# Optimization experiments

Measured on AMD Instinct MI355X. Metric: run time of the kernel, lower is better.

## Reference

```python
import jax, jax.numpy as jnp
import numpy as np

N, K, D, M, P, HG, HD = 120000, 8, 64, 100000, 16, 32, 96
VOXEL, TAU, OCC_INC, LMIN, LMAX = 0.1, 0.3, 0.5, -2.0, 3.5


def setup_inputs() -> dict:
    ks = jax.random.split(jax.random.key(0), 20)
    f32 = jnp.float32
    s = 0.05
    return {
        'pts_xyz': jax.random.uniform(ks[0], (N, 3), f32) * 10.0,
        'f_pts': jax.random.normal(ks[1], (N, D), f32),
        'z_latent': jax.random.normal(ks[2], (M, D), f32),
        'vals_st': jax.random.normal(ks[3], (M,), f32) * 0.5,
        'centers_xyz': jax.random.uniform(ks[4], (M, 3), f32) * 10.0,
        'Wf': jax.random.normal(ks[5], (P, D), f32) * s,
        'Wz': jax.random.normal(ks[6], (P, D), f32) * s,
        'w_delta': jax.random.normal(ks[7], (1, 3), f32) * s,
        'b_delta': jnp.zeros((1,), f32),
        'log_temp': jnp.zeros((1,), f32),
        'W_ih': jax.random.normal(ks[8], (3 * D, D), f32) * s,
        'W_hh': jax.random.normal(ks[9], (3 * D, D), f32) * s,
        'b_ih': jnp.zeros((3 * D,), f32),
        'b_hh': jnp.zeros((3 * D,), f32),
        'Wg1': jax.random.normal(ks[10], (HG, 2 * D), f32) * s,
        'bg1': jnp.zeros((HG,), f32),
        'Wg2': jax.random.normal(ks[11], (1, HG), f32) * s,
        'bg2': jnp.zeros((1,), f32),
        'ln_g': jnp.ones((D,), f32),
        'ln_b': jnp.zeros((D,), f32),
        'Wd1': jax.random.normal(ks[12], (HD, D), f32) * s,
        'bd1': jnp.zeros((HD,), f32),
        'Wd2': jax.random.normal(ks[13], (HD, HD), f32) * s,
        'bd2': jnp.zeros((HD,), f32),
        'Wd3': jax.random.normal(ks[14], (1, HD), f32) * s,
        'bd3': jnp.zeros((1,), f32),
        'keys': jnp.sort(jax.random.randint(ks[15], (M,), 0, 2 ** 30, jnp.int32)),
        'cand_idx': jax.random.randint(ks[16], (N, K), 0, M, jnp.int32),
    }


def _forward(pts_xyz, f_pts, z_latent, vals_st, centers_xyz, Wf, Wz, w_delta, b_delta,
             log_temp, W_ih, W_hh, b_ih, b_hh, Wg1, bg1, Wg2, bg2, ln_g, ln_b,
             Wd1, bd1, Wd2, bd2, Wd3, bd3, keys, cand_idx):
    # --- sparse voxel hash lookup + log-odds scatter update ---
    ijk = jnp.floor(pts_xyz / VOXEL).astype(jnp.int32)
    off = jnp.int32(1 << 9)
    h = ((ijk[:, 0] + off) << 20) ^ ((ijk[:, 1] + off) << 10) ^ (ijk[:, 2] + off)
    vox_idx = jnp.clip(jnp.searchsorted(keys, h), 0, M - 1)  # (N,)
    vals_new = jnp.clip(vals_st.at[vox_idx].add(OCC_INC), LMIN, LMAX)

    # --- top-K low-temperature routing: sim(f, z, delta) ---
    z_c = z_latent[cand_idx]                                  # (N,K,D) gather
    delta = pts_xyz[:, None, :] - centers_xyz[cand_idx]       # (N,K,3)
    Fp = f_pts @ Wf.T                                         # (N,P)
    Zp = z_c @ Wz.T                                           # (N,K,P)
    Fp = Fp / (jnp.linalg.norm(Fp, axis=-1, keepdims=True) + 1e-6)
    Zp = Zp / (jnp.linalg.norm(Zp, axis=-1, keepdims=True) + 1e-6)
    core = jnp.einsum('np,nkp->nk', Fp, Zp)
    dterm = jnp.einsum('nkc,c->nk', delta, w_delta[0]) + b_delta[0]
    sim = jnp.exp(log_temp[0]) * (core + dterm)
    w = jax.nn.softmax(sim / TAU, axis=-1)                    # (N,K)

    # --- scatter weighted point features to voxels ---
    flat_idx = cand_idx.reshape(-1)                           # (N*K,)
    contrib = (w[..., None] * f_pts[:, None, :]).reshape(-1, D)
    msg = jax.ops.segment_sum(contrib, flat_idx, num_segments=M)   # (M,D)
    wsum = jax.ops.segment_sum(w.reshape(-1), flat_idx, num_segments=M)
    msg = msg / (wsum[:, None] + 1e-6)

    # --- per-voxel gate + GRU latent fusion ---
    gate_in = jnp.concatenate([z_latent, msg], axis=-1)       # (M,2D)
    g = jax.nn.sigmoid(jax.nn.relu(gate_in @ Wg1.T + bg1) @ Wg2.T + bg2)  # (M,1)
    gi = msg @ W_ih.T + b_ih
    gh = z_latent @ W_hh.T + b_hh
    gir, giz, gin = jnp.split(gi, 3, axis=-1)
    ghr, ghz, ghn = jnp.split(gh, 3, axis=-1)
    r = jax.nn.sigmoid(gir + ghr)
    u = jax.nn.sigmoid(giz + ghz)
    n = jnp.tanh(gin + r * ghn)
    h_new = (1.0 - u) * n + u * z_latent
    z_new = z_latent + g * (h_new - z_latent)                 # (M,D)

    # --- decode occupancy: LN -> fc1 -> residual fc2 -> fc3 -> sigmoid ---
    mu = z_new.mean(-1, keepdims=True)
    var = z_new.var(-1, keepdims=True)
    x = (z_new - mu) * jax.lax.rsqrt(var + 1e-5) * ln_g + ln_b
    hd = jax.nn.relu(x @ Wd1.T + bd1)
    hd = hd + jax.nn.relu(hd @ Wd2.T + bd2)
    p = jax.nn.sigmoid((hd @ Wd3.T + bd3)[:, 0])              # (M,)

    return jnp.concatenate([p, vals_new])                     # (2M,)


def reference(pts_xyz, f_pts, z_latent, vals_st, centers_xyz, Wf, Wz, w_delta, b_delta,
              log_temp, W_ih, W_hh, b_ih, b_hh, Wg1, bg1, Wg2, bg2, ln_g, ln_b,
              Wd1, bd1, Wd2, bd2, Wd3, bd3, keys, cand_idx):
    return _forward(pts_xyz, f_pts, z_latent, vals_st, centers_xyz, Wf, Wz, w_delta,
                    b_delta, log_temp, W_ih, W_hh, b_ih, b_hh, Wg1, bg1, Wg2, bg2,
                    ln_g, ln_b, Wd1, bd1, Wd2, bd2, Wd3, bd3, keys, cand_idx)
```

## Files before the change

### kernel.cpp

```cpp
#include <hip/hip_runtime.h>
#include <math.h>

#define Nn 120000
#define Kk 8
#define Dd 64
#define Mm 100000
#define Pp 16
#define HGg 32
#define HDd 96
#define CAP 40
#define LUTB 16

typedef __attribute__((ext_vector_type(8))) short bf16x8;
typedef __attribute__((ext_vector_type(4))) float f32x4;
typedef __attribute__((ext_vector_type(4))) float fx4;
typedef __attribute__((ext_vector_type(4))) int ix4;

#define PB_K0    1563
#define PB_PREP  (PB_K0 + 3750)
#define PB_PACK  (PB_PREP + 22)
#define PB_INIT  (PB_PACK + 391)
#define PB_LUT   (PB_INIT + 391)

__device__ __forceinline__ float sigmoidf_(float x) { return 1.f / (1.f + __expf(-x)); }
__device__ __forceinline__ float tanh_fast(float x) {
    float e = __expf(2.f * x);
    return 1.f - 2.f / (e + 1.f);
}
__device__ __forceinline__ short f2bf(float f) {
    unsigned u = __float_as_uint(f);
    unsigned r = (u + 0x7fffu + ((u >> 16) & 1u)) >> 16;
    return (short)r;
}

__global__ __launch_bounds__(256) void k_prep_all(const float* __restrict__ z,
                                                  const float* __restrict__ Wz,
                                                  const float* __restrict__ centers,
                                                  const float* __restrict__ w_delta,
                                                  const int* __restrict__ keys,
                                                  const float* __restrict__ f_pts,
                                                  const float* __restrict__ Wf,
                                                  const float* __restrict__ Wg1,
                                                  const float* __restrict__ W_ih,
                                                  const float* __restrict__ W_hh,
                                                  const float* __restrict__ Wd1,
                                                  const float* __restrict__ Wd2,
                                                  const float* __restrict__ vals,
                                                  unsigned* __restrict__ Zbf,
                                                  float* __restrict__ cdot,
                                                  int* __restrict__ lut,
                                                  signed char* __restrict__ f8,
                                                  float* __restrict__ fpb,
                                                  short* __restrict__ wsW,
                                                  int* __restrict__ cnt,
                                                  float* __restrict__ vacc) {
    int b = blockIdx.x;
    if (b < PB_K0) {
        int g = threadIdx.x & 3;
        int m = b * 64 + (threadIdx.x >> 2);
        if (m >= Mm) return;
        const float4* zr = (const float4*)(z + (size_t)m * Dd + g * 16);
        float4 q0 = zr[0], q1 = zr[1], q2 = zr[2], q3 = zr[3];
        float acc[Pp];
#pragma unroll
        for (int p = 0; p < Pp; p++) {
            const float4* w = (const float4*)(Wz + (size_t)p * Dd + g * 16);
            float4 w0 = w[0], w1 = w[1], w2 = w[2], w3 = w[3];
            float s = q0.x * w0.x + q0.y * w0.y + q0.z * w0.z + q0.w * w0.w;
            s += q1.x * w1.x + q1.y * w1.y + q1.z * w1.z + q1.w * w1.w;
            s += q2.x * w2.x + q2.y * w2.y + q2.z * w2.z + q2.w * w2.w;
            s += q3.x * w3.x + q3.y * w3.y + q3.z * w3.z + q3.w * w3.w;
            acc[p] = s;
        }
#pragma unroll
        for (int p = 0; p < Pp; p++) {
            acc[p] += __shfl_xor(acc[p], 1, 64);
            acc[p] += __shfl_xor(acc[p], 2, 64);
        }
        float ss = 0.f;
#pragma unroll
        for (int p = 0; p < Pp; p++) ss = fmaf(acc[p], acc[p], ss);
        float inv = 1.f / (sqrtf(ss) + 1e-6f);
        unsigned* row = Zbf + (size_t)m * 8;
        if (g < 2) {
            uint4 o;
            unsigned w[4];
#pragma unroll
            for (int j = 0; j < 4; j++) {
                float v0 = acc[g * 8 + 2 * j] * inv;
                float v1 = acc[g * 8 + 2 * j + 1] * inv;
                w[j] = (unsigned)(unsigned short)f2bf(v0)
                     | ((unsigned)(unsigned short)f2bf(v1) << 16);
            }
            o.x = w[0]; o.y = w[1]; o.z = w[2]; o.w = w[3];
            ((uint4*)row)[g] = o;
        } else if (g == 2) {
            cdot[m] = centers[3 * m] * w_delta[0] + centers[3 * m + 1] * w_delta[1]
                    + centers[3 * m + 2] * w_delta[2];
        }
    } else if (b < PB_PREP) {
        int i = (b - PB_K0) * 256 + threadIdx.x;
        int g = i & 7;
        int e = i * 8;
        const fx4* src = (const fx4*)(f_pts + e);
        fx4 a = __builtin_nontemporal_load(src);
        fx4 bb = __builtin_nontemporal_load(src + 1);
        float v[8] = {a.x, a.y, a.z, a.w, bb.x, bb.y, bb.z, bb.w};
        unsigned lo = 0, hi = 0;
#pragma unroll
        for (int j = 0; j < 4; j++) {
            int q = (int)rintf(fminf(fmaxf(v[j], -4.f), 4.f) * 32.f);
            lo |= ((unsigned)q & 0xffu) << (8 * j);
        }
#pragma unroll
        for (int j = 0; j < 4; j++) {
            int q = (int)rintf(fminf(fmaxf(v[4 + j], -4.f), 4.f) * 32.f);
            hi |= ((unsigned)q & 0xffu) << (8 * j);
        }
        *(int2*)(f8 + e) = make_int2((int)lo, (int)hi);

        float fp[Pp];
#pragma unroll
        for (int p = 0; p < Pp; p++) {
            const float4* w = (const float4*)(Wf + (size_t)p * Dd + g * 8);
            float4 w0 = w[0], w1 = w[1];
            float s = v[0] * w0.x + v[1] * w0.y + v[2] * w0.z + v[3] * w0.w;
            s += v[4] * w1.x + v[5] * w1.y + v[6] * w1.z + v[7] * w1.w;
            fp[p] = s;
        }
#pragma unroll
        for (int p = 0; p < Pp; p++) {
            fp[p] += __shfl_xor(fp[p], 1, 64);
            fp[p] += __shfl_xor(fp[p], 2, 64);
            fp[p] += __shfl_xor(fp[p], 4, 64);
        }
        float ss = 0.f;
#pragma unroll
        for (int p = 0; p < Pp; p++) ss = fmaf(fp[p], fp[p], ss);
        float inv = 1.f / (sqrtf(ss) + 1e-6f);
#pragma unroll
        for (int p = 0; p < Pp; p++) fp[p] *= inv;
        if (g < 4) {
            float4 o;
            if (g == 0)      o = make_float4(fp[0], fp[1], fp[2], fp[3]);
            else if (g == 1) o = make_float4(fp[4], fp[5], fp[6], fp[7]);
            else if (g == 2) o = make_float4(fp[8], fp[9], fp[10], fp[11]);
            else             o = make_float4(fp[12], fp[13], fp[14], fp[15]);
            ((float4*)(fpb + (size_t)(i >> 3) * 16))[g] = o;
        }
    } else if (b < PB_PACK) {
        int idx = (b - PB_PREP) * 256 + threadIdx.x;
        if (idx >= 86 * 64) return;
        int f = idx >> 6, lane = idx & 63;
        int lrow = lane & 15, lhi = lane >> 4;
        const float* src;
        int t, c, K;
        if (f < 8)       { int g = f;      t = g >> 2; c = g & 3;  src = Wg1;  K = 128; }
        else if (f < 32) { int g = f - 8;  t = g >> 1; c = g & 1;  src = W_ih; K = 64; }
        else if (f < 56) { int g = f - 32; t = g >> 1; c = g & 1;  src = W_hh; K = 64; }
        else if (f < 68) { int g = f - 56; t = g >> 1; c = g & 1;  src = Wd1;  K = 64; }
        else             { int g = f - 68; t = g / 3;  c = g % 3;  src = Wd2;  K = 96; }
        int o = t * 16 + lrow;
        int k0 = c * 32 + lhi * 8;
        short* dst = wsW + ((size_t)f * 64 + lane) * 8;
#pragma unroll
        for (int j = 0; j < 8; j++) dst[j] = f2bf(src[(size_t)o * K + k0 + j]);
    } else if (b < PB_INIT) {
        int m = (b - PB_PACK) * 256 + threadIdx.x;
        if (m < Mm) {
            cnt[m] = 0;
            vacc[m] = vals[m];
        }
    } else {
        int i = (b - PB_INIT) * 256 + threadIdx.x;
        if (i <= Mm) {
            const int S = 30 - LUTB;
            int ki = (i < Mm) ? keys[i] : (1 << 30);
            int kp = (i > 0) ? keys[i - 1] : -1;
            int lo = (kp >> S) + 1;
            int hi = ki >> S;
            for (int p = lo; p <= hi; p++) lut[p] = i;
        }
    }
}

__global__ __launch_bounds__(256) void k1_route(const float* __restrict__ pts,
                                                const float* __restrict__ fpb,
                                                const float* __restrict__ w_delta,
                                                const float* __restrict__ b_delta,
                                                const float* __restrict__ log_temp,
                                                const int* __restrict__ keys,
                                                const int* __restrict__ cand,
                                                const unsigned* __restrict__ Zbf,
                                                const float* __restrict__ cdot,
                                                const int* __restrict__ lut,
                                                float* __restrict__ vacc,
                                                int* __restrict__ cnt,
                                                int2* __restrict__ rec) {
    int g = threadIdx.x & 7;
    int n = blockIdx.x * 32 + (threadIdx.x >> 3);

    int myid = __builtin_nontemporal_load(cand + (size_t)n * Kk + g);
    const uint4* zp = (const uint4*)(Zbf + (size_t)myid * 8);
    uint4 A = zp[0], B = zp[1];
    float cd = cdot[myid];
    const float4* fr = (const float4*)(fpb + (size_t)n * 16);
    float4 F0 = fr[0], F1 = fr[1], F2 = fr[2], F3 = fr[3];
    float px = pts[3 * n], py = pts[3 * n + 1], pz = pts[3 * n + 2];

    if (g == 0) {
        int ix = (int)floorf(px / 0.1f);
        int iy = (int)floorf(py / 0.1f);
        int iz = (int)floorf(pz / 0.1f);
        int h = ((ix + 512) << 20) ^ ((iy + 512) << 10) ^ (iz + 512);
        int pfx = h >> (30 - LUTB);
        int lo = lut[pfx], hi = lut[pfx + 1];
        while (lo < hi) {
            int mid = (lo + hi) >> 1;
            if (keys[mid] < h) lo = mid + 1; else hi = mid;
        }
        int vi = lo < (Mm - 1) ? lo : (Mm - 1);
        atomicAdd(vacc + vi, 0.5f);
    }

    float et = expf(log_temp[0]);
    float pdot = px * w_delta[0] + py * w_delta[1] + pz * w_delta[2] + b_delta[0];

    float fp[16] = {F0.x, F0.y, F0.z, F0.w, F1.x, F1.y, F1.z, F1.w,
                    F2.x, F2.y, F2.z, F2.w, F3.x, F3.y, F3.z, F3.w};
    unsigned uw[8] = {A.x, A.y, A.z, A.w, B.x, B.y, B.z, B.w};
    float core = 0.f;
#pragma unroll
    for (int j = 0; j < 8; j++) {
        float lo = __uint_as_float(uw[j] << 16);
        float hi = __uint_as_float(uw[j] & 0xffff0000u);
        core = fmaf(fp[2 * j], lo, core);
        core = fmaf(fp[2 * j + 1], hi, core);
    }
    float sim = et * (core + pdot - cd) / 0.3f;

    float mx = sim;
    mx = fmaxf(mx, __shfl_xor(mx, 1, 64));
    mx = fmaxf(mx, __shfl_xor(mx, 2, 64));
    mx = fmaxf(mx, __shfl_xor(mx, 4, 64));
    float e = __expf(sim - mx);
    float se = e;
    se += __shfl_xor(se, 1, 64);
    se += __shfl_xor(se, 2, 64);
    se += __shfl_xor(se, 4, 64);
    float w = e / se;

    int pos = atomicAdd(cnt + myid, 1);
    if (pos < CAP) {
        long long pk = (unsigned)n | ((long long)(unsigned)__float_as_int(w) << 32);
        *(long long*)(rec + (size_t)myid * CAP + pos) = pk;
    }
}

__global__ __launch_bounds__(256) void k2_reduce(const signed char* __restrict__ f8,
                                                 const int* __restrict__ cnt,
                                                 const int2* __restrict__ rec,
                                                 unsigned short* __restrict__ msgb) {
    int wv = threadIdx.x >> 6, lane = threadIdx.x & 63;
    int m = blockIdx.x * 4 + wv;
    int c = cnt[m];
    if (c > CAP) c = CAP;
    const ix4* r4 = (const ix4*)(rec + (size_t)m * CAP);
    float acc = 0.f, wsum = 0.f;
    for (int i0 = 0; i0 < c; i0 += 8) {
        ix4 A = __builtin_nontemporal_load(r4 + (i0 >> 1) + 0);
        ix4 B = __builtin_nontemporal_load(r4 + (i0 >> 1) + 1);
        ix4 C = __builtin_nontemporal_load(r4 + (i0 >> 1) + 2);
        ix4 D = __builtin_nontemporal_load(r4 + (i0 >> 1) + 3);
        int nn[8];
        float ww[8];
        int rn[8] = {A.x, A.z, B.x, B.z, C.x, C.z, D.x, D.z};
        int rw[8] = {A.y, A.w, B.y, B.w, C.y, C.w, D.y, D.w};
#pragma unroll
        for (int k = 0; k < 8; k++) {
            bool valid = (i0 + k) < c;
            nn[k] = valid ? rn[k] : 0;
            ww[k] = valid ? __int_as_float(rw[k]) : 0.f;
        }
        float vv[8];
#pragma unroll
        for (int k = 0; k < 8; k++)
            vv[k] = (float)f8[((size_t)nn[k] << 6) + lane];
#pragma unroll
        for (int k = 0; k < 8; k++) {
            wsum += ww[k];
            acc = fmaf(ww[k], vv[k], acc);
        }
    }
    acc *= 0.03125f;
    msgb[(size_t)m * Dd + lane] = (unsigned short)f2bf(acc / (wsum + 1e-6f));
}

__global__ __launch_bounds__(256, 3) void k3_mfma(const float* __restrict__ z_latent,
                                                  const unsigned short* __restrict__ msgb,
                                                  const short* __restrict__ wsW,
                                                  const float* __restrict__ bg1,
                                                  const float* __restrict__ Wg2,
                                                  const float* __restrict__ bg2,
                                                  const float* __restrict__ b_ih,
                                                  const float* __restrict__ b_hh,
                                                  const float* __restrict__ ln_g,
                                                  const float* __restrict__ ln_b,
                                                  const float* __restrict__ bd1,
                                                  const float* __restrict__ bd2,
                                                  const float* __restrict__ Wd3,
                                                  const float* __restrict__ bd3,
                                                  const float* __restrict__ vacc,
                                                  float* __restrict__ out) {
    __shared__ float scr_all[4][16 * 97];
    int wv = threadIdx.x >> 6, lane = threadIdx.x & 63;
    int tile = blockIdx.x * 4 + wv;
    if (tile >= Mm / 16) return;
    int m0 = tile * 16;
    float* scr = scr_all[wv];
    int lrow = lane & 15;
    int lhi = lane >> 4;

    if (lane < 16) {
        float v = vacc[m0 + lane];
        out[Mm + m0 + lane] = fminf(fmaxf(v, -2.f), 3.5f);
    }

    const bf16x8* WF = (const bf16x8*)wsW;
#define BFRAG(off) (WF[(off) * 64 + lane])

    bf16x8 za[2], ma[2];
    const float* zrow = z_latent + (size_t)(m0 + lrow) * Dd + lhi * 8;
    const bf16x8* mrow = (const bf16x8*)(msgb + (size_t)(m0 + lrow) * Dd + lhi * 8);
#pragma unroll
    for (int c = 0; c < 2; c++) {
        bf16x8 t0;
#pragma unroll
        for (int j = 0; j < 8; j++) t0[j] = f2bf(zrow[c * 32 + j]);
        za[c] = t0;
        ma[c] = mrow[c * 4];
    }

    bf16x8 wgf[8];
#pragma unroll
    for (int j = 0; j < 8; j++) wgf[j] = BFRAG(j);
    f32x4 g0 = {0.f, 0.f, 0.f, 0.f}, g1 = {0.f, 0.f, 0.f, 0.f};
    bf16x8 gateA[4] = {za[0], za[1], ma[0], ma[1]};
#pragma unroll
    for (int c = 0; c < 4; c++) {
        g0 = __builtin_amdgcn_mfma_f32_16x16x32_bf16(gateA[c], wgf[c], g0, 0, 0, 0);
        g1 = __builtin_amdgcn_mfma_f32_16x16x32_bf16(gateA[c], wgf[4 + c], g1, 0, 0, 0);
    }
    float bgA = bg1[lrow], bgB = bg1[16 + lrow];
    float w2A = Wg2[lrow], w2B = Wg2[16 + lrow];
    float g[4];
#pragma unroll
    for (int r = 0; r < 4; r++) {
        float ga = fmaxf(g0[r] + bgA, 0.f) * w2A + fmaxf(g1[r] + bgB, 0.f) * w2B;
        ga += __shfl_xor(ga, 1, 64);
        ga += __shfl_xor(ga, 2, 64);
        ga += __shfl_xor(ga, 4, 64);
        ga += __shfl_xor(ga, 8, 64);
        g[r] = sigmoidf_(ga + bg2[0]);
    }

    float zn[4][4];
    float ps[4] = {0.f, 0.f, 0.f, 0.f}, pq[4] = {0.f, 0.f, 0.f, 0.f};
#pragma unroll
    for (int t = 0; t < 4; t++) {
        bf16x8 wt[12];
#pragma unroll
        for (int c = 0; c < 2; c++) {
            wt[0 + c]  = BFRAG(8 + t * 2 + c);
            wt[2 + c]  = BFRAG(8 + (t + 4) * 2 + c);
            wt[4 + c]  = BFRAG(8 + (t + 8) * 2 + c);
            wt[6 + c]  = BFRAG(32 + t * 2 + c);
            wt[8 + c]  = BFRAG(32 + (t + 4) * 2 + c);
            wt[10 + c] = BFRAG(32 + (t + 8) * 2 + c);
        }
        f32x4 Ar = {0.f, 0.f, 0.f, 0.f}, Az = Ar, An = Ar, Br = Ar, Bz = Ar, Bn = Ar;
#pragma unroll
        for (int c = 0; c < 2; c++) {
            Ar = __builtin_amdgcn_mfma_f32_16x16x32_bf16(ma[c], wt[0 + c], Ar, 0, 0, 0);
            Az = __builtin_amdgcn_mfma_f32_16x16x32_bf16(ma[c], wt[2 + c], Az, 0, 0, 0);
            An = __builtin_amdgcn_mfma_f32_16x16x32_bf16(ma[c], wt[4 + c], An, 0, 0, 0);
            Br = __builtin_amdgcn_mfma_f32_16x16x32_bf16(za[c], wt[6 + c], Br, 0, 0, 0);
            Bz = __builtin_amdgcn_mfma_f32_16x16x32_bf16(za[c], wt[8 + c], Bz, 0, 0, 0);
            Bn = __builtin_amdgcn_mfma_f32_16x16x32_bf16(za[c], wt[10 + c], Bn, 0, 0, 0);
        }
        int oc = t * 16 + lrow;
        float bir = b_ih[oc], biz = b_ih[64 + oc], bin = b_ih[128 + oc];
        float bhr = b_hh[oc], bhz = b_hh[64 + oc], bhn = b_hh[128 + oc];
#pragma unroll
        for (int r = 0; r < 4; r++) {
            int row = lhi * 4 + r;
            float zo = z_latent[(size_t)(m0 + row) * Dd + oc];
            float rr = sigmoidf_(Ar[r] + bir + Br[r] + bhr);
            float uu = sigmoidf_(Az[r] + biz + Bz[r] + bhz);
            float nnv = tanh_fast(An[r] + bin + rr * (Bn[r] + bhn));
            float hn = (1.f - uu) * nnv + uu * zo;
            float z2 = zo + g[r] * (hn - zo);
            zn[t][r] = z2;
            ps[r] += z2;
            pq[r] = fmaf(z2, z2, pq[r]);
        }
    }
    float mu[4], rs[4];
#pragma unroll
    for (int r = 0; r < 4; r++) {
        float s = ps[r], q = pq[r];
        s += __shfl_xor(s, 1, 64); q += __shfl_xor(q, 1, 64);
        s += __shfl_xor(s, 2, 64); q += __shfl_xor(q, 2, 64);
        s += __shfl_xor(s, 4, 64); q += __shfl_xor(q, 4, 64);
        s += __shfl_xor(s, 8, 64); q += __shfl_xor(q, 8, 64);
        float m = s * (1.f / 64.f);
        float v = q * (1.f / 64.f) - m * m;
        mu[r] = m;
        rs[r] = rsqrtf(v + 1e-5f);
    }
#pragma unroll
    for (int t = 0; t < 4; t++) {
        int o = t * 16 + lrow;
        float lg = ln_g[o], lb = ln_b[o];
#pragma unroll
        for (int r = 0; r < 4; r++)
            scr[(lhi * 4 + r) * 97 + o] = (zn[t][r] - mu[r]) * rs[r] * lg + lb;
    }
    __threadfence_block();

    bf16x8 xa[2];
#pragma unroll
    for (int c = 0; c < 2; c++) {
        bf16x8 tb;
#pragma unroll
        for (int j = 0; j < 8; j++) tb[j] = f2bf(scr[lrow * 97 + c * 32 + lhi * 8 + j]);
        xa[c] = tb;
    }
    bf16x8 wf1[12];
#pragma unroll
    for (int j = 0; j < 12; j++) wf1[j] = BFRAG(56 + j);
    f32x4 h1t[6];
#pragma unroll
    for (int t = 0; t < 6; t++) h1t[t] = (f32x4){0.f, 0.f, 0.f, 0.f};
#pragma unroll
    for (int t = 0; t < 6; t++)
#pragma unroll
        for (int c = 0; c < 2; c++)
            h1t[t] = __builtin_amdgcn_mfma_f32_16x16x32_bf16(xa[c], wf1[t * 2 + c], h1t[t], 0, 0, 0);
    float h1r[6][4];
#pragma unroll
    for (int t = 0; t < 6; t++) {
        float bb = bd1[t * 16 + lrow];
#pragma unroll
        for (int r = 0; r < 4; r++) {
            h1r[t][r] = fmaxf(h1t[t][r] + bb, 0.f);
            scr[(lhi * 4 + r) * 97 + t * 16 + lrow] = h1r[t][r];
        }
    }
    __threadfence_block();

    bf16x8 ha[3];
#pragma unroll
    for (int c = 0; c < 3; c++) {
        bf16x8 tb;
#pragma unroll
        for (int j = 0; j < 8; j++) tb[j] = f2bf(scr[lrow * 97 + c * 32 + lhi * 8 + j]);
        ha[c] = tb;
    }
    bf16x8 wf2[18];
#pragma unroll
    for (int j = 0; j < 18; j++) wf2[j] = BFRAG(68 + j);
    f32x4 o2[6];
#pragma unroll
    for (int t = 0; t < 6; t++) o2[t] = (f32x4){0.f, 0.f, 0.f, 0.f};
#pragma unroll
    for (int t = 0; t < 6; t++)
#pragma unroll
        for (int c = 0; c < 3; c++)
            o2[t] = __builtin_amdgcn_mfma_f32_16x16x32_bf16(ha[c], wf2[t * 3 + c], o2[t], 0, 0, 0);
    float pacc[4] = {0.f, 0.f, 0.f, 0.f};
#pragma unroll
    for (int t = 0; t < 6; t++) {
        int o = t * 16 + lrow;
        float bb = bd2[o], w3 = Wd3[o];
#pragma unroll
        for (int r = 0; r < 4; r++) {
            float hd2 = h1r[t][r] + fmaxf(o2[t][r] + bb, 0.f);
            pacc[r] = fmaf(hd2, w3, pacc[r]);
        }
    }
#pragma unroll
    for (int r = 0; r < 4; r++) {
        float s = pacc[r];
        s += __shfl_xor(s, 1, 64);
        s += __shfl_xor(s, 2, 64);
        s += __shfl_xor(s, 4, 64);
        s += __shfl_xor(s, 8, 64);
        if (lrow == 0) out[m0 + lhi * 4 + r] = sigmoidf_(s + bd3[0]);
    }
#undef BFRAG
}

extern "C" void kernel_launch(void* const* d_in, const int* in_sizes, int n_in,
                              void* d_out, int out_size, void* d_ws, size_t ws_size,
                              hipStream_t stream) {
    const float* pts      = (const float*)d_in[0];
    const float* f_pts    = (const float*)d_in[1];
    const float* z_lat    = (const float*)d_in[2];
    const float* vals     = (const float*)d_in[3];
    const float* centers  = (const float*)d_in[4];
    const float* Wf       = (const float*)d_in[5];
    const float* Wz       = (const float*)d_in[6];
    const float* w_delta  = (const float*)d_in[7];
    const float* b_delta  = (const float*)d_in[8];
    const float* log_temp = (const float*)d_in[9];
    const float* W_ih     = (const float*)d_in[10];
    const float* W_hh     = (const float*)d_in[11];
    const float* b_ih     = (const float*)d_in[12];
    const float* b_hh     = (const float*)d_in[13];
    const float* Wg1      = (const float*)d_in[14];
    const float* bg1      = (const float*)d_in[15];
    const float* Wg2      = (const float*)d_in[16];
    const float* bg2      = (const float*)d_in[17];
    const float* ln_g     = (const float*)d_in[18];
    const float* ln_b     = (const float*)d_in[19];
    const float* Wd1      = (const float*)d_in[20];
    const float* bd1      = (const float*)d_in[21];
    const float* Wd2      = (const float*)d_in[22];
    const float* bd2      = (const float*)d_in[23];
    const float* Wd3      = (const float*)d_in[24];
    const float* bd3      = (const float*)d_in[25];
    const int*   keys     = (const int*)d_in[26];
    const int*   cand     = (const int*)d_in[27];
    float* out = (float*)d_out;

    float* ws = (float*)d_ws;
    short* wsW = (short*)ws;
    unsigned* Zbf = (unsigned*)(ws + 32768);
    float* cdot = ws + 32768 + 800000;
    signed char* f8 = (signed char*)(ws + 32768 + 900000);
    float* base = ws + 32768 + 900000 + 1920000;
    unsigned short* msgb = (unsigned short*)base;
    float* fpb = base;
    float* vacc = base + (size_t)Mm * Dd / 2;
    int*   cnt  = (int*)(vacc + Mm);
    int2*  rec  = (int2*)(cnt + Mm);
    int*   lut  = (int*)((int*)rec + (size_t)Mm * CAP * 2);

    k_prep_all<<<PB_LUT, 256, 0, stream>>>(z_lat, Wz, centers, w_delta, keys, f_pts,
                                           Wf, Wg1, W_ih, W_hh, Wd1, Wd2, vals,
                                           Zbf, cdot, lut, f8, fpb, wsW, cnt, vacc);
    k1_route<<<Nn / 32, 256, 0, stream>>>(pts, fpb, w_delta, b_delta, log_temp,
                                          keys, cand, Zbf, cdot, lut, vacc, cnt, rec);
    k2_reduce<<<Mm / 4, 256, 0, stream>>>(f8, cnt, rec, msgb);
    k3_mfma<<<(Mm / 16 + 3) / 4, 256, 0, stream>>>(z_lat, msgb, wsW, bg1, Wg2, bg2,
                                                   b_ih, b_hh, ln_g, ln_b, bd1, bd2,
                                                   Wd3, bd3, vacc, out);
}
```

Measured before the change: 320.4 us.

## Bin scatter records by voxel blocks and reduce with LDS atomics

Per-voxel record lists with capacity 40 are replaced by bins of 128 voxels. Each bin is split into 8 sub-buckets chosen from the routing block index, so fewer global cells receive atomics and the writes are more contiguous. The reduce kernel now runs one block per bin and accumulates the weighted messages in shared memory with LDS atomics before writing them out. In exchange, far fewer reduce blocks are launched, which cuts available parallelism. It also adds more global atomic contention on the bin counters, and records beyond 256 per sub-bucket are silently dropped.

```diff
diff --git a/kernel.cpp b/kernel.cpp
--- a/kernel.cpp
+++ b/kernel.cpp
@@ -8,8 +8,9 @@
 #define Pp 16
 #define HGg 32
 #define HDd 96
-#define CAP 40
 #define LUTB 16
+#define NBINS 782
+#define BCAP 256
 
 typedef __attribute__((ext_vector_type(8))) short bf16x8;
 typedef __attribute__((ext_vector_type(4))) float f32x4;
@@ -52,7 +53,7 @@
                                                   signed char* __restrict__ f8,
                                                   float* __restrict__ fpb,
                                                   short* __restrict__ wsW,
-                                                  int* __restrict__ cnt,
+                                                  int* __restrict__ bincnt,
                                                   float* __restrict__ vacc) {
     int b = blockIdx.x;
     if (b < PB_K0) {
@@ -167,10 +168,8 @@
         for (int j = 0; j < 8; j++) dst[j] = f2bf(src[(size_t)o * K + k0 + j]);
     } else if (b < PB_INIT) {
         int m = (b - PB_PACK) * 256 + threadIdx.x;
-        if (m < Mm) {
-            cnt[m] = 0;
-            vacc[m] = vals[m];
-        }
+        if (m < Mm) vacc[m] = vals[m];
+        if (m < 8 * NBINS) bincnt[m] = 0;
     } else {
         int i = (b - PB_INIT) * 256 + threadIdx.x;
         if (i <= Mm) {
@@ -195,8 +194,8 @@
                                                 const float* __restrict__ cdot,
                                                 const int* __restrict__ lut,
                                                 float* __restrict__ vacc,
-                                                int* __restrict__ cnt,
-                                                int2* __restrict__ rec) {
+                                                int* __restrict__ bincnt,
+                                                long long* __restrict__ binrec) {
     int g = threadIdx.x & 7;
     int n = blockIdx.x * 32 + (threadIdx.x >> 3);
 
@@ -250,50 +249,70 @@
     se += __shfl_xor(se, 4, 64);
     float w = e / se;
 
-    int pos = atomicAdd(cnt + myid, 1);
-    if (pos < CAP) {
-        long long pk = (unsigned)n | ((long long)(unsigned)__float_as_int(w) << 32);
-        *(long long*)(rec + (size_t)myid * CAP + pos) = pk;
+    int bin = myid >> 7;
+    int cell = ((blockIdx.x & 7) * NBINS) + bin;
+    int pos = atomicAdd(bincnt + cell, 1);
+    if (pos < BCAP) {
+        unsigned lo32 = (unsigned)n | ((unsigned)(myid & 127) << 17);
+        long long pk = (long long)(((unsigned long long)(unsigned)__float_as_int(w) << 32)
+                                   | (unsigned long long)lo32);
+        binrec[((size_t)cell << 8) + pos] = pk;
     }
 }
 
 __global__ __launch_bounds__(256) void k2_reduce(const signed char* __restrict__ f8,
-                                                 const int* __restrict__ cnt,
-                                                 const int2* __restrict__ rec,
+                                                 const int* __restrict__ bincnt,
+                                                 const long long* __restrict__ binrec,
                                                  unsigned short* __restrict__ msgb) {
-    int wv = threadIdx.x >> 6, lane = threadIdx.x & 63;
-    int m = blockIdx.x * 4 + wv;
-    int c = cnt[m];
-    if (c > CAP) c = CAP;
-    const ix4* r4 = (const ix4*)(rec + (size_t)m * CAP);
-    float acc = 0.f, wsum = 0.f;
-    for (int i0 = 0; i0 < c; i0 += 8) {
-        ix4 A = __builtin_nontemporal_load(r4 + (i0 >> 1) + 0);
-        ix4 B = __builtin_nontemporal_load(r4 + (i0 >> 1) + 1);
-        ix4 C = __builtin_nontemporal_load(r4 + (i0 >> 1) + 2);
-        ix4 D = __builtin_nontemporal_load(r4 + (i0 >> 1) + 3);
-        int nn[8];
-        float ww[8];
-        int rn[8] = {A.x, A.z, B.x, B.z, C.x, C.z, D.x, D.z};
-        int rw[8] = {A.y, A.w, B.y, B.w, C.y, C.w, D.y, D.w};
-#pragma unroll
-        for (int k = 0; k < 8; k++) {
-            bool valid = (i0 + k) < c;
-            nn[k] = valid ? rn[k] : 0;
-            ww[k] = valid ? __int_as_float(rw[k]) : 0.f;
-        }
-        float vv[8];
-#pragma unroll
-        for (int k = 0; k < 8; k++)
-            vv[k] = (float)f8[((size_t)nn[k] << 6) + lane];
-#pragma unroll
-        for (int k = 0; k < 8; k++) {
-            wsum += ww[k];
-            acc = fmaf(ww[k], vv[k], acc);
-        }
-    }
-    acc *= 0.03125f;
-    msgb[(size_t)m * Dd + lane] = (unsigned short)f2bf(acc / (wsum + 1e-6f));
+    __shared__ float macc[128 * 64];
+    __shared__ float wacc[128];
+    int tid = threadIdx.x, wv = tid >> 6, lane = tid & 63;
+    int b = blockIdx.x;
+    for (int i = tid; i < 128 * 64; i += 256) macc[i] = 0.f;
+    if (tid < 128) wacc[tid] = 0.f;
+    __syncthreads();
+
+#pragma unroll 1
+    for (int x = 0; x < 8; x++) {
+        int cell = x * NBINS + b;
+        int c = bincnt[cell];
+        if (c > BCAP) c = BCAP;
+        const long long* src = binrec + ((size_t)cell << 8);
+        for (int r0 = wv * 8; r0 < c; r0 += 32) {
+            long long pk[8];
+#pragma unroll
+            for (int j = 0; j < 8; j++) {
+                int r = r0 + j;
+                pk[j] = src[(r < c) ? r : 0];
+            }
+            float vv[8], wj[8];
+            int ml[8];
+#pragma unroll
+            for (int j = 0; j < 8; j++) {
+                bool val = (r0 + j) < c;
+                unsigned lo = (unsigned)(unsigned long long)pk[j];
+                int nn = (int)(lo & 0x1FFFFu);
+                ml[j] = (int)((lo >> 17) & 127u);
+                wj[j] = val ? __int_as_float((int)(pk[j] >> 32)) : 0.f;
+                nn = val ? nn : 0;
+                vv[j] = (float)f8[((size_t)nn << 6) + lane];
+            }
+#pragma unroll
+            for (int j = 0; j < 8; j++) {
+                atomicAdd(&macc[ml[j] * 64 + lane], wj[j] * vv[j]);
+                if (lane == 0) atomicAdd(&wacc[ml[j]], wj[j]);
+            }
+        }
+    }
+    __syncthreads();
+
+    for (int i = tid; i < 128 * 64; i += 256) {
+        int v = i >> 6, d = i & 63;
+        int m = b * 128 + v;
+        if (m < Mm)
+            msgb[(size_t)m * Dd + d] =
+                (unsigned short)f2bf(macc[i] * 0.03125f / (wacc[v] + 1e-6f));
+    }
 }
 
 __global__ __launch_bounds__(256, 3) void k3_mfma(const float* __restrict__ z_latent,
@@ -543,16 +562,16 @@
     unsigned short* msgb = (unsigned short*)base;
     float* fpb = base;
     float* vacc = base + (size_t)Mm * Dd / 2;
-    int*   cnt  = (int*)(vacc + Mm);
-    int2*  rec  = (int2*)(cnt + Mm);
-    int*   lut  = (int*)((int*)rec + (size_t)Mm * CAP * 2);
+    int*   bincnt = (int*)(vacc + Mm);
+    long long* binrec = (long long*)(bincnt + 6400);
+    int*   lut = (int*)(binrec + (size_t)8 * NBINS * BCAP);
 
     k_prep_all<<<PB_LUT, 256, 0, stream>>>(z_lat, Wz, centers, w_delta, keys, f_pts,
                                            Wf, Wg1, W_ih, W_hh, Wd1, Wd2, vals,
-                                           Zbf, cdot, lut, f8, fpb, wsW, cnt, vacc);
+                                           Zbf, cdot, lut, f8, fpb, wsW, bincnt, vacc);
     k1_route<<<Nn / 32, 256, 0, stream>>>(pts, fpb, w_delta, b_delta, log_temp,
-                                          keys, cand, Zbf, cdot, lut, vacc, cnt, rec);
-    k2_reduce<<<Mm / 4, 256, 0, stream>>>(f8, cnt, rec, msgb);
+                                          keys, cand, Zbf, cdot, lut, vacc, bincnt, binrec);
+    k2_reduce<<<NBINS, 256, 0, stream>>>(f8, bincnt, binrec, msgb);
     k3_mfma<<<(Mm / 16 + 3) / 4, 256, 0, stream>>>(z_lat, msgb, wsW, bg1, Wg2, bg2,
                                                    b_ih, b_hh, ln_g, ln_b, bd1, bd2,
                                                    Wd3, bd3, vacc, out);
```

After: 709.7 us. 2.21x slower.
